# Kernel tuning notes

Measured on AMD Instinct MI355X. Metric: run time of the kernel, lower is better.

The kernel has to match this reference:

```python
import jax, jax.numpy as jnp
import numpy as np
from functools import partial

C = 256
N_HEADS = 8
OFFSET_RANGE = 2.0


def _dwconv(x, w):
    # depthwise conv, SAME padding; w: (C,1,k,k)
    c = x.shape[1]
    return jax.lax.conv_general_dilated(
        x, w, window_strides=(1, 1), padding='SAME',
        feature_group_count=c, dimension_numbers=('NCHW', 'OIHW', 'NCHW'))


def _grid_sample_bilinear(x, gx, gy):
    # x: (B,C,H,W); gx,gy: (B,H,W) normalized in [-1,1]; align_corners=True
    B, Cc, H, W = x.shape
    ix = (gx + 1.0) * 0.5 * (W - 1)
    iy = (gy + 1.0) * 0.5 * (H - 1)
    x0f = jnp.floor(ix)
    y0f = jnp.floor(iy)
    fx = (ix - x0f)[:, None, :, :].reshape(B, 1, H * W)
    fy = (iy - y0f)[:, None, :, :].reshape(B, 1, H * W)
    x0 = jnp.clip(x0f.astype(jnp.int32), 0, W - 1)
    x1 = jnp.clip(x0 + 1, 0, W - 1)
    y0 = jnp.clip(y0f.astype(jnp.int32), 0, H - 1)
    y1 = jnp.clip(y0 + 1, 0, H - 1)
    xf = x.reshape(B, Cc, H * W)

    def gather(yi, xi):
        idx = (yi * W + xi).reshape(B, H * W)
        return jax.vmap(lambda f, i: f[:, i])(xf, idx)  # (B,C,N)

    v00 = gather(y0, x0)
    v01 = gather(y0, x1)
    v10 = gather(y1, x0)
    v11 = gather(y1, x1)
    out = (v00 * (1 - fx) * (1 - fy) + v01 * fx * (1 - fy)
           + v10 * (1 - fx) * fy + v11 * fx * fy)
    return out.reshape(B, Cc, H, W)


def setup_inputs() -> dict:
    key = jax.random.key(0)
    ks = jax.random.split(key, 11)
    B, H, W = 1, 64, 64
    s = 0.05
    return {
        'x': jax.random.normal(ks[0], (B, C, H, W), jnp.float32),
        'offset_weights': jnp.ones((3,), jnp.float32) + 0.1 * jax.random.normal(ks[1], (3,)),
        'w3': s * jax.random.normal(ks[2], (C, 1, 3, 3), jnp.float32),
        'w5': s * jax.random.normal(ks[3], (C, 1, 5, 5), jnp.float32),
        'w7': s * jax.random.normal(ks[4], (C, 1, 7, 7), jnp.float32),
        'w_offproj': s * jax.random.normal(ks[5], (2, C), jnp.float32),
        'wq': s * jax.random.normal(ks[6], (C, C), jnp.float32),
        'wk': s * jax.random.normal(ks[7], (C, C), jnp.float32),
        'wv': s * jax.random.normal(ks[8], (C, C), jnp.float32),
        'wo': s * jax.random.normal(ks[9], (C, C), jnp.float32),
        'beta': jnp.asarray(0.5, jnp.float32),
    }


def reference(x, offset_weights, w3, w5, w7, w_offproj, wq, wk, wv, wo, beta):
    B, Cc, H, W = x.shape
    head_dim = Cc // N_HEADS
    scale = head_dim ** -0.5
    N = H * W

    # multi-scale depthwise offset features
    off_feat = (_dwconv(x, w3) * offset_weights[0]
                + _dwconv(x, w5) * offset_weights[1]
                + _dwconv(x, w7) * offset_weights[2])
    offset = jnp.einsum('oc,bchw->bohw', w_offproj, jax.nn.relu(off_feat))  # (B,2,H,W) = (y,x)

    # reference points: ((i+0.5)/(size-1))*2 - 1
    ref_y = ((jnp.arange(H, dtype=jnp.float32) + 0.5) / (H - 1.0)) * 2.0 - 1.0
    ref_x = ((jnp.arange(W, dtype=jnp.float32) + 0.5) / (W - 1.0)) * 2.0 - 1.0
    gy = jnp.clip(ref_y[None, :, None] + jnp.tanh(offset[:, 0]) * OFFSET_RANGE, -1.0, 1.0)
    gx = jnp.clip(ref_x[None, None, :] + jnp.tanh(offset[:, 1]) * OFFSET_RANGE, -1.0, 1.0)
    x_sampled = _grid_sample_bilinear(x, gx, gy)

    # Manhattan decay bias
    yy = jnp.repeat(jnp.arange(H), W)
    xx = jnp.tile(jnp.arange(W), H)
    dist = (jnp.abs(yy[:, None] - yy[None, :]) + jnp.abs(xx[:, None] - xx[None, :])).astype(jnp.float32)
    decay = jnp.exp(-dist / (jnp.abs(beta) + 1e-6))  # (N,N)

    q = jnp.einsum('oc,bchw->bohw', wq, x).reshape(B, N_HEADS, head_dim, N)
    k = jnp.einsum('oc,bchw->bohw', wk, x_sampled).reshape(B, N_HEADS, head_dim, N)
    v = jnp.einsum('oc,bchw->bohw', wv, x_sampled).reshape(B, N_HEADS, head_dim, N)

    attn = jnp.einsum('bhdn,bhdm->bhnm', q, k) * scale + decay[None, None]
    attn = jax.nn.softmax(attn, axis=-1)
    out = jnp.einsum('bhnm,bhdm->bhdn', attn, v).reshape(B, Cc, H, W)
    return jnp.einsum('oc,bchw->bohw', wo, out)
```

## Files before the change

### kernel.cpp

```cpp
#include <hip/hip_runtime.h>
#include <hip/hip_bf16.h>


typedef __bf16 bf16x8 __attribute__((ext_vector_type(8)));
typedef float f32x4 __attribute__((ext_vector_type(4)));

__device__ __forceinline__ f32x4 mfma16(bf16x8 a, bf16x8 b, f32x4 c) {
    return __builtin_amdgcn_mfma_f32_16x16x32_bf16(a, b, c, 0, 0, 0);
}

__device__ __forceinline__ unsigned pack_bf16(float pa, float pb) {
    return __builtin_amdgcn_perm(__float_as_uint(pb), __float_as_uint(pa), 0x07060302u);
}

__device__ __forceinline__ float fast_tanh(float x) {
    const float t = __builtin_amdgcn_exp2f(x * 2.8853900817779268f);
    return (t - 1.0f) * __builtin_amdgcn_rcpf(t + 1.0f);
}

__global__ void prep_transpose_kernel(const float* __restrict__ x, float* __restrict__ xTf,
                                      __hip_bfloat16* __restrict__ xTb,
                                      const float* __restrict__ w3, const float* __restrict__ w5,
                                      const float* __restrict__ w7, const float* __restrict__ ow,
                                      const float* __restrict__ wq, const float* __restrict__ wk,
                                      const float* __restrict__ wv, const float* __restrict__ wo,
                                      float* __restrict__ wcomb, __hip_bfloat16* __restrict__ wb) {
    __shared__ float tile[32][33];
    const int b = blockIdx.x;
    if (b < 1024) {
        const int p0 = (b >> 3) * 32, c0 = (b & 7) * 32;
        const int tx = threadIdx.x & 31, ty = threadIdx.x >> 5;
#pragma unroll
        for (int i = 0; i < 4; ++i)
            tile[ty + i * 8][tx] = x[(size_t)(c0 + ty + i * 8) * 4096 + p0 + tx];
        __syncthreads();
#pragma unroll
        for (int i = 0; i < 4; ++i) {
            const float v = tile[tx][ty + i * 8];
            const size_t o = (size_t)(p0 + ty + i * 8) * 256 + c0 + tx;
            xTf[o] = v;
            xTb[o] = __float2bfloat16(v);
        }
    } else if (b < 1073) {
        const int i = b - 1024, c = threadIdx.x;
        const int dy = i / 7, dx = i % 7;
        float val = ow[2] * w7[c * 49 + i];
        if (dy >= 1 && dy <= 5 && dx >= 1 && dx <= 5)
            val += ow[1] * w5[c * 25 + (dy - 1) * 5 + (dx - 1)];
        if (dy >= 2 && dy <= 4 && dx >= 2 && dx <= 4)
            val += ow[0] * w3[c * 9 + (dy - 2) * 3 + (dx - 2)];
        wcomb[i * 256 + c] = val;
    } else {
        const int idx = (b - 1073) * 256 + threadIdx.x;
        const int m = idx >> 16;
        const float* src = (m == 0) ? wq : (m == 1) ? wk : (m == 2) ? wv : wo;
        const float sc = (m == 0) ? 0.25507535f : 1.0f;
        wb[idx] = __float2bfloat16(src[idx & 65535] * sc);
    }
}

__global__ __launch_bounds__(256) void sample_kernel(
    const float* __restrict__ xTf, const float* __restrict__ wcomb,
    const float* __restrict__ wop, __hip_bfloat16* __restrict__ xsT) {
    const int b = blockIdx.x;
    const int y = b >> 3;
    const int x0 = (b & 7) * 8;
    const int c = threadIdx.x;

    float wc[49];
#pragma unroll
    for (int i = 0; i < 49; ++i) wc[i] = wcomb[i * 256 + c];

    float acc[8];
#pragma unroll
    for (int px = 0; px < 8; ++px) acc[px] = 0.f;

#pragma unroll
    for (int dy = 0; dy < 7; ++dy) {
        const int yy = y + dy - 3;
        if (yy < 0 || yy > 63) continue;
        float v[14];
#pragma unroll
        for (int j = 0; j < 14; ++j) {
            const int xx = x0 - 3 + j;
            v[j] = (xx >= 0 && xx <= 63) ? xTf[(size_t)(yy * 64 + xx) * 256 + c] : 0.f;
        }
#pragma unroll
        for (int px = 0; px < 8; ++px)
#pragma unroll
            for (int dx = 0; dx < 7; ++dx)
                acc[px] = fmaf(v[px + dx], wc[dy * 7 + dx], acc[px]);
    }

    const float wy = wop[c], wx = wop[256 + c];
    float s[16];
#pragma unroll
    for (int px = 0; px < 8; ++px) {
        const float r = fmaxf(acc[px], 0.f);
        s[px] = wy * r;
        s[8 + px] = wx * r;
    }
#pragma unroll
    for (int off = 1; off < 64; off <<= 1)
#pragma unroll
        for (int i = 0; i < 16; ++i) s[i] += __shfl_xor(s[i], off, 64);

    __shared__ float red[4][16];
    const int lane = c & 63, wid = c >> 6;
    if (lane == 0)
#pragma unroll
        for (int i = 0; i < 16; ++i) red[wid][i] = s[i];
    __syncthreads();

#pragma unroll
    for (int px = 0; px < 8; ++px) {
        const float offy = red[0][px] + red[1][px] + red[2][px] + red[3][px];
        const float offx = red[0][8 + px] + red[1][8 + px] + red[2][8 + px] + red[3][8 + px];
        const int pxa = x0 + px;
        const float refy = ((y + 0.5f) / 63.0f) * 2.0f - 1.0f;
        const float refx = ((pxa + 0.5f) / 63.0f) * 2.0f - 1.0f;
        const float gy = fminf(fmaxf(refy + fast_tanh(offy) * 2.0f, -1.0f), 1.0f);
        const float gx = fminf(fmaxf(refx + fast_tanh(offx) * 2.0f, -1.0f), 1.0f);
        const float iy = (gy + 1.0f) * 31.5f;
        const float ix = (gx + 1.0f) * 31.5f;
        const float y0f = floorf(iy), x0f = floorf(ix);
        const float fy = iy - y0f, fx = ix - x0f;
        int yi0 = min(max((int)y0f, 0), 63), xi0 = min(max((int)x0f, 0), 63);
        int yi1 = min(yi0 + 1, 63), xi1 = min(xi0 + 1, 63);
        const float v00 = xTf[(size_t)(yi0 * 64 + xi0) * 256 + c];
        const float v01 = xTf[(size_t)(yi0 * 64 + xi1) * 256 + c];
        const float v10 = xTf[(size_t)(yi1 * 64 + xi0) * 256 + c];
        const float v11 = xTf[(size_t)(yi1 * 64 + xi1) * 256 + c];
        const float out = v00 * (1.f - fx) * (1.f - fy) + v01 * fx * (1.f - fy) +
                          v10 * (1.f - fx) * fy + v11 * fx * fy;
        xsT[(size_t)(y * 64 + pxa) * 256 + c] = __float2bfloat16(out);
    }
}

template <typename OutT>
__device__ __forceinline__ void gemm_body(const __hip_bfloat16* A, const __hip_bfloat16* B,
                                          OutT* out, int ldc, int m0, int n0) {
    const int w = threadIdx.x >> 6, lane = threadIdx.x & 63;
    const int g = lane >> 4, c = lane & 15;
    f32x4 acc[4];
#pragma unroll
    for (int nt = 0; nt < 4; ++nt) acc[nt] = (f32x4){0.f, 0.f, 0.f, 0.f};
    const __hip_bfloat16* Ar = A + (size_t)(m0 + w * 16 + c) * 256 + g * 8;
#pragma unroll
    for (int kc = 0; kc < 8; ++kc) {
        const bf16x8 a = *reinterpret_cast<const bf16x8*>(Ar + kc * 32);
#pragma unroll
        for (int nt = 0; nt < 4; ++nt) {
            const bf16x8 b = *reinterpret_cast<const bf16x8*>(
                B + (size_t)(n0 + nt * 16 + c) * 256 + kc * 32 + g * 8);
            acc[nt] = mfma16(a, b, acc[nt]);
        }
    }
#pragma unroll
    for (int nt = 0; nt < 4; ++nt)
#pragma unroll
        for (int r = 0; r < 4; ++r) {
            const size_t o = (size_t)(m0 + w * 16 + 4 * g + r) * ldc + n0 + nt * 16 + c;
            if constexpr (__is_same(OutT, float)) out[o] = acc[nt][r];
            else out[o] = __float2bfloat16(acc[nt][r]);
        }
}

__global__ __launch_bounds__(256) void gemm_qkv(const __hip_bfloat16* __restrict__ xq,
                                                const __hip_bfloat16* __restrict__ xs,
                                                const __hip_bfloat16* __restrict__ wb,
                                                __hip_bfloat16* __restrict__ q_t,
                                                __hip_bfloat16* __restrict__ k_t,
                                                __hip_bfloat16* __restrict__ vv) {
    const int z = blockIdx.z;
    if (z == 0)
        gemm_body<__hip_bfloat16>(xq, wb, q_t, 256, blockIdx.x * 64, blockIdx.y * 64);
    else if (z == 1)
        gemm_body<__hip_bfloat16>(xs, wb + 65536, k_t, 256, blockIdx.x * 64, blockIdx.y * 64);
    else
        gemm_body<__hip_bfloat16>(wb + 2 * 65536, xs, vv, 4096, blockIdx.y * 64,
                                  blockIdx.x * 64);
}

template <typename OutT>
__global__ __launch_bounds__(256) void gemm_abt(const __hip_bfloat16* __restrict__ A,
                                                const __hip_bfloat16* __restrict__ B,
                                                OutT* __restrict__ out, int ldc) {
    gemm_body<OutT>(A, B, out, ldc, blockIdx.x * 64, blockIdx.y * 64);
}

__global__ __launch_bounds__(256, 2) void attn_kernel(
    const __hip_bfloat16* __restrict__ q_t,
    const __hip_bfloat16* __restrict__ k_t,
    const __hip_bfloat16* __restrict__ vv,
    const float* __restrict__ beta_p,
    __hip_bfloat16* __restrict__ att)
{
    __shared__ __align__(16) char smem[37888];
    const int h = blockIdx.x & 7;
    const int nb = blockIdx.x >> 3;
    const int n0 = nb * 64;
    const int tid = threadIdx.x;
    const int w = tid >> 6, lane = tid & 63, g = lane >> 4, c = lane & 15;

    const float bta = fabsf(beta_p[0]) + 1e-6f;
    const float L2E = 1.4426950408889634f;
    const float c2 = L2E / bta;

    float d64d[7][4];
#pragma unroll
    for (int dlt = 0; dlt < 7; ++dlt)
#pragma unroll
        for (int r = 0; r < 4; ++r) {
            const int dd = 16 * (dlt - 3) + c - 4 * g - r;
            d64d[dlt][r] = L2E * __builtin_amdgcn_exp2f(-c2 * fabsf((float)dd));
        }

    bf16x8 aq[4];
#pragma unroll
    for (int nt = 0; nt < 4; ++nt)
        aq[nt] = *reinterpret_cast<const bf16x8*>(
            q_t + (size_t)(n0 + nt * 16 + c) * 256 + h * 32 + g * 8);

    f32x4 o_acc[4][2];
    float l_part[4] = {0.f, 0.f, 0.f, 0.f};
#pragma unroll
    for (int nt = 0; nt < 4; ++nt) {
        o_acc[nt][0] = (f32x4){0.f, 0.f, 0.f, 0.f};
        o_acc[nt][1] = (f32x4){0.f, 0.f, 0.f, 0.f};
    }

    uint2* pl = (uint2*)smem + w * 1024;
    const int wbi = g * 16 + c;
    const int rb = (g >> 1) * 64 + (g & 1) * 32 + c;
    const f32x4 zf = (f32x4){0.f, 0.f, 0.f, 0.f};

    auto loadK = [&](int it, bf16x8* bk) {
        const size_t m0 = (size_t)(it * 4 + w) * 64;
#pragma unroll
        for (int mt = 0; mt < 4; ++mt)
            bk[mt] = *reinterpret_cast<const bf16x8*>(
                k_t + (m0 + mt * 16 + c) * 256 + h * 32 + g * 8);
    };
    auto body = [&](int it, bf16x8* bk) {
        const int ym = it * 4 + w;
        const size_t m0 = (size_t)ym * 64;
        bf16x8 bv[2][2];
#pragma unroll
        for (int dt = 0; dt < 2; ++dt)
#pragma unroll
            for (int mc = 0; mc < 2; ++mc)
                bv[dt][mc] = *reinterpret_cast<const bf16x8*>(
                    vv + (size_t)(h * 32 + dt * 16 + c) * 4096 + m0 + mc * 32 + g * 8);

        const int ady = nb > ym ? nb - ym : ym - nb;
        if (ady >= 4) {
#pragma unroll
            for (int nt = 0; nt < 4; ++nt) {
                f32x4 s[4];
#pragma unroll
                for (int mt = 0; mt < 4; ++mt) s[mt] = mfma16(bk[mt], aq[nt], zf);
#pragma unroll
                for (int mt = 0; mt < 4; ++mt) {
                    float p[4];
#pragma unroll
                    for (int r = 0; r < 4; ++r)
                        p[r] = __builtin_amdgcn_exp2f(s[mt][r]);
                    l_part[nt] += (p[0] + p[1]) + (p[2] + p[3]);
                    pl[wbi + (nt * 4 + mt) * 64] = uint2{pack_bf16(p[0], p[1]),
                                                         pack_bf16(p[2], p[3])};
                }
            }
        } else {
            const float a2 = __builtin_amdgcn_exp2f(-c2 * (float)ady);
#pragma unroll
            for (int nt = 0; nt < 4; ++nt) {
                f32x4 s[4];
#pragma unroll
                for (int mt = 0; mt < 4; ++mt) s[mt] = mfma16(bk[mt], aq[nt], zf);
#pragma unroll
                for (int mt = 0; mt < 4; ++mt) {
                    float p[4];
#pragma unroll
                    for (int r = 0; r < 4; ++r)
                        p[r] = __builtin_amdgcn_exp2f(fmaf(a2, d64d[nt - mt + 3][r], s[mt][r]));
                    l_part[nt] += (p[0] + p[1]) + (p[2] + p[3]);
                    pl[wbi + (nt * 4 + mt) * 64] = uint2{pack_bf16(p[0], p[1]),
                                                         pack_bf16(p[2], p[3])};
                }
            }
        }
#pragma unroll
        for (int nt = 0; nt < 4; ++nt)
#pragma unroll
            for (int mc = 0; mc < 2; ++mc) {
                const int idx = rb + (nt * 4 + 2 * mc) * 64;
                union { uint2 u[2]; bf16x8 v; } t;
                t.u[0] = pl[idx];
                t.u[1] = pl[idx + 16];
                o_acc[nt][0] = mfma16(t.v, bv[0][mc], o_acc[nt][0]);
                o_acc[nt][1] = mfma16(t.v, bv[1][mc], o_acc[nt][1]);
            }
    };

    bf16x8 bkA[4], bkB[4];
    loadK(0, bkA);
#pragma unroll 1
    for (int it2 = 0; it2 < 8; ++it2) {
        loadK(2 * it2 + 1, bkB);
        body(2 * it2, bkA);
        if (it2 < 7) loadK(2 * it2 + 2, bkA);
        body(2 * it2 + 1, bkB);
    }

#pragma unroll
    for (int nt = 0; nt < 4; ++nt) {
        float v = l_part[nt];
        v += __shfl_xor(v, 16);
        v += __shfl_xor(v, 32);
        l_part[nt] = v;
    }

    __syncthreads();
    float* ob = (float*)smem;
    float* lred = (float*)(smem + 36864);
#pragma unroll
    for (int nt = 0; nt < 4; ++nt) {
        if (g == 0) lred[w * 64 + nt * 16 + c] = l_part[nt];
#pragma unroll
        for (int r = 0; r < 4; ++r) {
            const int row = 16 * nt + 4 * g + r;
            ob[w * 2304 + row * 36 + c] = o_acc[nt][0][r];
            ob[w * 2304 + row * 36 + 16 + c] = o_acc[nt][1][r];
        }
    }
    __syncthreads();

#pragma unroll
    for (int k = 0; k < 8; ++k) {
        const int flat = k * 256 + tid;
        const int row = flat >> 5, d = flat & 31;
        const float O = ob[row * 36 + d] + ob[2304 + row * 36 + d] +
                        ob[4608 + row * 36 + d] + ob[6912 + row * 36 + d];
        const float L = lred[row] + lred[64 + row] + lred[128 + row] + lred[192 + row];
        att[(size_t)(n0 + row) * 256 + h * 32 + d] = __float2bfloat16(O / L);
    }
}

extern "C" void kernel_launch(void* const* d_in, const int* in_sizes, int n_in,
                              void* d_out, int out_size, void* d_ws, size_t ws_size,
                              hipStream_t stream) {
    (void)in_sizes; (void)n_in; (void)out_size; (void)ws_size;
    const float* x    = (const float*)d_in[0];
    const float* ow   = (const float*)d_in[1];
    const float* w3   = (const float*)d_in[2];
    const float* w5   = (const float*)d_in[3];
    const float* w7   = (const float*)d_in[4];
    const float* wop  = (const float*)d_in[5];
    const float* wq   = (const float*)d_in[6];
    const float* wk   = (const float*)d_in[7];
    const float* wv   = (const float*)d_in[8];
    const float* wo   = (const float*)d_in[9];
    const float* beta = (const float*)d_in[10];

    char* ws = (char*)d_ws;
    const size_t MB = 1 << 20;
    float*          xTf = (float*)(ws);
    __hip_bfloat16* xTb = (__hip_bfloat16*)(ws + 4 * MB);
    __hip_bfloat16* xsT = (__hip_bfloat16*)(ws + 6 * MB);
    __hip_bfloat16* q_t = (__hip_bfloat16*)(ws + 8 * MB);
    __hip_bfloat16* k_t = (__hip_bfloat16*)(ws + 10 * MB);
    __hip_bfloat16* vv  = (__hip_bfloat16*)(ws + 12 * MB);
    __hip_bfloat16* att = (__hip_bfloat16*)(ws + 14 * MB);
    __hip_bfloat16* wb  = (__hip_bfloat16*)(ws + 16 * MB);
    float* wcomb        = (float*)(ws + 16 * MB + 512 * 1024);
    __hip_bfloat16* wob = wb + 3 * 65536;

    prep_transpose_kernel<<<2097, 256, 0, stream>>>(x, xTf, xTb, w3, w5, w7, ow,
                                                    wq, wk, wv, wo, wcomb, wb);
    sample_kernel<<<512, 256, 0, stream>>>(xTf, wcomb, wop, xsT);
    gemm_qkv<<<dim3(64, 4, 3), 256, 0, stream>>>(xTb, xsT, wb, q_t, k_t, vv);
    attn_kernel<<<512, 256, 0, stream>>>(q_t, k_t, vv, beta, att);
    gemm_abt<float><<<dim3(4, 64), 256, 0, stream>>>(wob, att, (float*)d_out, 4096);
}
```

Measured before the change: 147.3 us.

## Split attention over key halves and add a combine kernel

The attention kernel now splits the key dimension into two halves, which doubles the grid to 1024 blocks. Each block writes unnormalized partial outputs and row sums to workspace, and a new combine kernel sums them and normalizes. The change also drops the software-pipelined double-buffered K loads and the precomputed decay table, recomputing the decay bias with an extra exp per element to cut register use. The aim is better occupancy and load balance across CUs, at the cost of an extra launch, extra global traffic for fp32 partials, and more transcendental work.

```diff
diff --git a/kernel.cpp b/kernel.cpp
--- a/kernel.cpp
+++ b/kernel.cpp
@@ -194,11 +194,13 @@
     const __hip_bfloat16* __restrict__ k_t,
     const __hip_bfloat16* __restrict__ vv,
     const float* __restrict__ beta_p,
-    __hip_bfloat16* __restrict__ att)
+    float* __restrict__ opart,
+    float* __restrict__ lpart)
 {
     __shared__ __align__(16) char smem[37888];
     const int h = blockIdx.x & 7;
-    const int nb = blockIdx.x >> 3;
+    const int half = (blockIdx.x >> 3) & 1;
+    const int nb = blockIdx.x >> 4;
     const int n0 = nb * 64;
     const int tid = threadIdx.x;
     const int w = tid >> 6, lane = tid & 63, g = lane >> 4, c = lane & 15;
@@ -206,15 +208,7 @@
     const float bta = fabsf(beta_p[0]) + 1e-6f;
     const float L2E = 1.4426950408889634f;
     const float c2 = L2E / bta;
-
-    float d64d[7][4];
-#pragma unroll
-    for (int dlt = 0; dlt < 7; ++dlt)
-#pragma unroll
-        for (int r = 0; r < 4; ++r) {
-            const int dd = 16 * (dlt - 3) + c - 4 * g - r;
-            d64d[dlt][r] = L2E * __builtin_amdgcn_exp2f(-c2 * fabsf((float)dd));
-        }
+    const float base = (float)(c - 4 * g);
 
     bf16x8 aq[4];
 #pragma unroll
@@ -235,16 +229,15 @@
     const int rb = (g >> 1) * 64 + (g & 1) * 32 + c;
     const f32x4 zf = (f32x4){0.f, 0.f, 0.f, 0.f};
 
-    auto loadK = [&](int it, bf16x8* bk) {
-        const size_t m0 = (size_t)(it * 4 + w) * 64;
+#pragma unroll 1
+    for (int it = 0; it < 8; ++it) {
+        const int ym = half * 32 + it * 4 + w;
+        const size_t m0 = (size_t)ym * 64;
+        bf16x8 bk[4];
 #pragma unroll
         for (int mt = 0; mt < 4; ++mt)
             bk[mt] = *reinterpret_cast<const bf16x8*>(
                 k_t + (m0 + mt * 16 + c) * 256 + h * 32 + g * 8);
-    };
-    auto body = [&](int it, bf16x8* bk) {
-        const int ym = it * 4 + w;
-        const size_t m0 = (size_t)ym * 64;
         bf16x8 bv[2][2];
 #pragma unroll
         for (int dt = 0; dt < 2; ++dt)
@@ -272,7 +265,7 @@
                 }
             }
         } else {
-            const float a2 = __builtin_amdgcn_exp2f(-c2 * (float)ady);
+            const float ab = L2E * __builtin_amdgcn_exp2f(-c2 * (float)ady);
 #pragma unroll
             for (int nt = 0; nt < 4; ++nt) {
                 f32x4 s[4];
@@ -282,8 +275,11 @@
                 for (int mt = 0; mt < 4; ++mt) {
                     float p[4];
 #pragma unroll
-                    for (int r = 0; r < 4; ++r)
-                        p[r] = __builtin_amdgcn_exp2f(fmaf(a2, d64d[nt - mt + 3][r], s[mt][r]));
+                    for (int r = 0; r < 4; ++r) {
+                        const float dd = fabsf((float)(16 * (nt - mt)) + base - (float)r);
+                        const float bias = ab * __builtin_amdgcn_exp2f(-c2 * dd);
+                        p[r] = __builtin_amdgcn_exp2f(s[mt][r] + bias);
+                    }
                     l_part[nt] += (p[0] + p[1]) + (p[2] + p[3]);
                     pl[wbi + (nt * 4 + mt) * 64] = uint2{pack_bf16(p[0], p[1]),
                                                          pack_bf16(p[2], p[3])};
@@ -301,16 +297,6 @@
                 o_acc[nt][0] = mfma16(t.v, bv[0][mc], o_acc[nt][0]);
                 o_acc[nt][1] = mfma16(t.v, bv[1][mc], o_acc[nt][1]);
             }
-    };
-
-    bf16x8 bkA[4], bkB[4];
-    loadK(0, bkA);
-#pragma unroll 1
-    for (int it2 = 0; it2 < 8; ++it2) {
-        loadK(2 * it2 + 1, bkB);
-        body(2 * it2, bkA);
-        if (it2 < 7) loadK(2 * it2 + 2, bkA);
-        body(2 * it2 + 1, bkB);
     }
 
 #pragma unroll
@@ -342,9 +328,26 @@
         const int row = flat >> 5, d = flat & 31;
         const float O = ob[row * 36 + d] + ob[2304 + row * 36 + d] +
                         ob[4608 + row * 36 + d] + ob[6912 + row * 36 + d];
-        const float L = lred[row] + lred[64 + row] + lred[128 + row] + lred[192 + row];
-        att[(size_t)(n0 + row) * 256 + h * 32 + d] = __float2bfloat16(O / L);
-    }
+        opart[(size_t)half * 1048576 + (size_t)(n0 + row) * 256 + h * 32 + d] = O;
+        if (d == 0) {
+            const float L = lred[row] + lred[64 + row] + lred[128 + row] + lred[192 + row];
+            lpart[(size_t)(half * 8 + h) * 4096 + n0 + row] = L;
+        }
+    }
+}
+
+__global__ __launch_bounds__(256) void combine_kernel(const float* __restrict__ opart,
+                                                      const float* __restrict__ lpart,
+                                                      __hip_bfloat16* __restrict__ att) {
+    const int i = (blockIdx.x * 256 + threadIdx.x) * 4;
+    const int n = i >> 8, cc = i & 255, h = cc >> 5;
+    const float4 o0 = *reinterpret_cast<const float4*>(opart + i);
+    const float4 o1 = *reinterpret_cast<const float4*>(opart + 1048576 + i);
+    const float L = lpart[(size_t)h * 4096 + n] + lpart[(size_t)(8 + h) * 4096 + n];
+    const float invL = __builtin_amdgcn_rcpf(L);
+    const float b0 = (o0.x + o1.x) * invL, b1 = (o0.y + o1.y) * invL;
+    const float b2 = (o0.z + o1.z) * invL, b3 = (o0.w + o1.w) * invL;
+    *reinterpret_cast<uint2*>(att + i) = uint2{pack_bf16(b0, b1), pack_bf16(b2, b3)};
 }
 
 extern "C" void kernel_launch(void* const* d_in, const int* in_sizes, int n_in,
@@ -365,21 +368,24 @@
 
     char* ws = (char*)d_ws;
     const size_t MB = 1 << 20;
-    float*          xTf = (float*)(ws);
-    __hip_bfloat16* xTb = (__hip_bfloat16*)(ws + 4 * MB);
-    __hip_bfloat16* xsT = (__hip_bfloat16*)(ws + 6 * MB);
-    __hip_bfloat16* q_t = (__hip_bfloat16*)(ws + 8 * MB);
-    __hip_bfloat16* k_t = (__hip_bfloat16*)(ws + 10 * MB);
-    __hip_bfloat16* vv  = (__hip_bfloat16*)(ws + 12 * MB);
-    __hip_bfloat16* att = (__hip_bfloat16*)(ws + 14 * MB);
-    __hip_bfloat16* wb  = (__hip_bfloat16*)(ws + 16 * MB);
-    float* wcomb        = (float*)(ws + 16 * MB + 512 * 1024);
-    __hip_bfloat16* wob = wb + 3 * 65536;
+    float*          xTf   = (float*)(ws);
+    __hip_bfloat16* xTb   = (__hip_bfloat16*)(ws + 4 * MB);
+    __hip_bfloat16* xsT   = (__hip_bfloat16*)(ws + 6 * MB);
+    __hip_bfloat16* q_t   = (__hip_bfloat16*)(ws + 8 * MB);
+    __hip_bfloat16* k_t   = (__hip_bfloat16*)(ws + 10 * MB);
+    __hip_bfloat16* vv    = (__hip_bfloat16*)(ws + 12 * MB);
+    float*          opart = (float*)(ws + 14 * MB);
+    float*          lpart = (float*)(ws + 22 * MB);
+    __hip_bfloat16* att   = (__hip_bfloat16*)(ws + 23 * MB);
+    __hip_bfloat16* wb    = (__hip_bfloat16*)(ws + 25 * MB);
+    float* wcomb          = (float*)(ws + 25 * MB + 512 * 1024);
+    __hip_bfloat16* wob   = wb + 3 * 65536;
 
     prep_transpose_kernel<<<2097, 256, 0, stream>>>(x, xTf, xTb, w3, w5, w7, ow,
                                                     wq, wk, wv, wo, wcomb, wb);
     sample_kernel<<<512, 256, 0, stream>>>(xTf, wcomb, wop, xsT);
     gemm_qkv<<<dim3(64, 4, 3), 256, 0, stream>>>(xTb, xsT, wb, q_t, k_t, vv);
-    attn_kernel<<<512, 256, 0, stream>>>(q_t, k_t, vv, beta, att);
+    attn_kernel<<<1024, 256, 0, stream>>>(q_t, k_t, vv, beta, opart, lpart);
+    combine_kernel<<<1024, 256, 0, stream>>>(opart, lpart, att);
     gemm_abt<float><<<dim3(4, 64), 256, 0, stream>>>(wob, att, (float*)d_out, 4096);
 }
```

After: 151.4 us. +2.8%, slower.
